# Kernel optimization log

Measured on AMD Instinct MI355X. Metric: run time of the kernel, lower is better.

## Reference

```python
import jax, jax.numpy as jnp
import numpy as np

NUM_EXPERTS = 64
TOP_K = 8
ALPHA = 0.001


def setup_inputs() -> dict:
    key = jax.random.key(0)
    k1, k2 = jax.random.split(key)
    hidden_states = jax.random.normal(k1, (16384, 2048), dtype=jnp.float32)
    # nn.Linear(D, E) weight has shape (E, D); init ~ N(0, 1/sqrt(D))
    weight = jax.random.normal(k2, (NUM_EXPERTS, 2048), dtype=jnp.float32) / jnp.sqrt(2048.0)
    return {"hidden_states": hidden_states, "weight": weight}


def reference(hidden_states, weight):
    # Router logits: (N, E)
    logits = jnp.einsum("nd,ed->ne", hidden_states, weight)
    scores = jax.nn.softmax(logits, axis=-1)

    # top-k (lax.top_k returns sorted values; torch used sorted=False, same set)
    topk_weights, topk_indices = jax.lax.top_k(scores, TOP_K)  # (N, K)
    topk_weights = topk_weights / jnp.sum(topk_weights, axis=-1, keepdims=True)

    # Aux load-balancing loss (training path). Instead of materializing a
    # (N, K, E) one-hot tensor, count tokens per expert with a scatter-add.
    num_tokens = hidden_states.shape[0]
    counts = jnp.zeros((NUM_EXPERTS,), dtype=jnp.float32).at[topk_indices.ravel()].add(1.0)
    tokens_per_expert = counts / (num_tokens * TOP_K)
    mean_prob = jnp.mean(scores, axis=0)  # (E,)
    aux_loss = ALPHA * NUM_EXPERTS * jnp.sum(tokens_per_expert * mean_prob)

    return topk_weights, topk_indices, aux_loss
```

## Files before the change

kernel.cpp:

```cpp
#include <hip/hip_runtime.h>
#include <hip/hip_bf16.h>

#define N_TOKENS 16384
#define DIM      2048
#define NEXP     64
#define TOPK     8
#define LOSCALE  2048.0f
#define NBLOCKS  512
#define TOKPB    32
#define LSTRIDE  66
#define NREP     32
#define NCHUNKS  64
#define NROUNDS  16
#define SROW     264

typedef _Float16 half8   __attribute__((ext_vector_type(8)));
typedef float    floatx4 __attribute__((ext_vector_type(4)));

__global__ __launch_bounds__(256) void wprep_kernel(const float* __restrict__ W,
                                                    _Float16* __restrict__ Whi,
                                                    _Float16* __restrict__ Wlo) {
    int i = blockIdx.x * 256 + threadIdx.x;
    float w = W[i];
    _Float16 h = (_Float16)w;
    Whi[i] = h;
    Wlo[i] = (_Float16)((w - (float)h) * LOSCALE);
}

__device__ __forceinline__ void split2x8(const float4& f0, const float4& f1,
                                         half8& H, half8& L) {
    float v[8] = {f0.x, f0.y, f0.z, f0.w, f1.x, f1.y, f1.z, f1.w};
    #pragma unroll
    for (int j = 0; j < 8; ++j) {
        _Float16 h = (_Float16)v[j];
        H[j] = h;
        L[j] = (_Float16)((v[j] - (float)h) * LOSCALE);
    }
}

__device__ __forceinline__ void split_write(_Float16* sw,
                                            const float4& f0, const float4& f1,
                                            const float4& f2, const float4& f3) {
    half8 h, l;
    split2x8(f0, f1, h, l);
    *(half8*)(sw)      = h;
    *(half8*)(sw + 8)  = l;
    split2x8(f2, f3, h, l);
    *(half8*)(sw + 16) = h;
    *(half8*)(sw + 24) = l;
}

__global__ __launch_bounds__(256) void moe_kernel(const float* __restrict__ A,
                                                  const _Float16* __restrict__ Whi,
                                                  const _Float16* __restrict__ Wlo,
                                                  float* __restrict__ out_w,
                                                  float* __restrict__ out_i,
                                                  float* __restrict__ out_aux,
                                                  float* __restrict__ cnt_ws,
                                                  float* __restrict__ sp_ws,
                                                  unsigned int* __restrict__ ticket) {
    __shared__ _Float16 stage[2][TOKPB][SROW];
    __shared__ float    xch[TOKPB * LSTRIDE];
    __shared__ float    s_cnt[NEXP];
    __shared__ float    s_sp[NEXP];
    __shared__ int      s_last;

    const int tid   = threadIdx.x;
    const int lane  = tid & 63;
    const int wv    = tid >> 6;
    const int row16 = lane & 15;
    const int quad  = lane >> 4;
    const int tbase = blockIdx.x * TOKPB;

    if (tid < NEXP) { s_cnt[tid] = 0.f; s_sp[tid] = 0.f; }

    const int srow = tid >> 3;
    const int sseg = tid & 7;
    const float* Ap = A + (size_t)(tbase + srow) * DIM + sseg * 16;
    _Float16* sw0 = &stage[0][0][0] + srow * SROW + (2 * sseg) * 16;
    _Float16* sw1 = &stage[1][0][0] + srow * SROW + (2 * sseg) * 16;

    const _Float16* bhp = Whi + (size_t)(wv * 16 + row16) * DIM + quad * 8;
    const _Float16* blp = Wlo + (size_t)(wv * 16 + row16) * DIM + quad * 8;

    floatx4 acc0[2] = {};
    floatx4 acc1[2] = {};

#define BODY(I_, BH_, BL_)                                                    \
    do {                                                                      \
        int _off = row16 * SROW + ((I_) * 4 + quad) * 16;                     \
        half8 _a0 = *(const half8*)(sb + _off);                               \
        half8 _l0 = *(const half8*)(sb + _off + 8);                           \
        half8 _a1 = *(const half8*)(sb + _off + 16 * SROW);                   \
        half8 _l1 = *(const half8*)(sb + _off + 16 * SROW + 8);               \
        acc0[0] = __builtin_amdgcn_mfma_f32_16x16x32_f16(_a0, BH_, acc0[0], 0, 0, 0); \
        acc1[0] = __builtin_amdgcn_mfma_f32_16x16x32_f16(_a0, BL_, acc1[0], 0, 0, 0); \
        acc1[0] = __builtin_amdgcn_mfma_f32_16x16x32_f16(_l0, BH_, acc1[0], 0, 0, 0); \
        acc0[1] = __builtin_amdgcn_mfma_f32_16x16x32_f16(_a1, BH_, acc0[1], 0, 0, 0); \
        acc1[1] = __builtin_amdgcn_mfma_f32_16x16x32_f16(_a1, BL_, acc1[1], 0, 0, 0); \
        acc1[1] = __builtin_amdgcn_mfma_f32_16x16x32_f16(_l1, BH_, acc1[1], 0, 0, 0); \
    } while (0)

    half8 b0h = *(const half8*)(bhp + 0 * 32), b0l = *(const half8*)(blp + 0 * 32);
    half8 b1h = *(const half8*)(bhp + 1 * 32), b1l = *(const half8*)(blp + 1 * 32);
    half8 b2h = *(const half8*)(bhp + 2 * 32), b2l = *(const half8*)(blp + 2 * 32);
    half8 b3h = *(const half8*)(bhp + 3 * 32), b3l = *(const half8*)(blp + 3 * 32);

    {
        float4 f0 = *(const float4*)(Ap + 0);
        float4 f1 = *(const float4*)(Ap + 4);
        float4 f2 = *(const float4*)(Ap + 8);
        float4 f3 = *(const float4*)(Ap + 12);
        split_write(sw0, f0, f1, f2, f3);
    }
    __syncthreads();

    for (int r = 0; r < NROUNDS; ++r) {
        float4 g0, g1, g2, g3;
        if (r < NROUNDS - 1) {
            const float* p = Ap + (r + 1) * 128;
            g0 = *(const float4*)(p);
            g1 = *(const float4*)(p + 4);
            g2 = *(const float4*)(p + 8);
            g3 = *(const float4*)(p + 12);
        }
        const _Float16* sb = &stage[r & 1][0][0];
        const int c = 4 * r;

        BODY(0, b0h, b0l);
        if (c + 4 < NCHUNKS) { b0h = *(const half8*)(bhp + (c + 4) * 32); b0l = *(const half8*)(blp + (c + 4) * 32); }
        BODY(1, b1h, b1l);
        if (c + 5 < NCHUNKS) { b1h = *(const half8*)(bhp + (c + 5) * 32); b1l = *(const half8*)(blp + (c + 5) * 32); }
        BODY(2, b2h, b2l);
        if (c + 6 < NCHUNKS) { b2h = *(const half8*)(bhp + (c + 6) * 32); b2l = *(const half8*)(blp + (c + 6) * 32); }
        BODY(3, b3h, b3l);
        if (c + 7 < NCHUNKS) { b3h = *(const half8*)(bhp + (c + 7) * 32); b3l = *(const half8*)(blp + (c + 7) * 32); }

        if (r < NROUNDS - 1) split_write((r & 1) ? sw0 : sw1, g0, g1, g2, g3);
        __syncthreads();
    }

    const float inv = 1.0f / LOSCALE;
    #pragma unroll
    for (int mt = 0; mt < 2; ++mt)
        #pragma unroll
        for (int reg = 0; reg < 4; ++reg) {
            int tok = mt * 16 + quad * 4 + reg;
            xch[tok * LSTRIDE + wv * 16 + row16] = acc0[mt][reg] + acc1[mt][reg] * inv;
        }
    __syncthreads();

    float sp = 0.f, cnt = 0.f;
    for (int i = 0; i < 8; ++i) {
        int t = wv * 8 + i;
        float lg = xch[t * LSTRIDE + lane];

        float m = lg;
        #pragma unroll
        for (int off = 32; off; off >>= 1) m = fmaxf(m, __shfl_xor(m, off));
        float e = expf(lg - m);
        float ssum = e;
        #pragma unroll
        for (int off = 32; off; off >>= 1) ssum += __shfl_xor(ssum, off);
        float score = e / ssum;
        sp += score;

        int rank = 0;
        #pragma unroll
        for (int j = 0; j < 64; ++j) {
            float sj = __shfl(score, j);
            rank += (sj > score) || (sj == score && j < lane);
        }
        bool sel = rank < TOPK;

        float v = sel ? score : 0.f;
        #pragma unroll
        for (int off = 32; off; off >>= 1) v += __shfl_xor(v, off);

        if (sel) {
            out_w[(size_t)(tbase + t) * TOPK + rank] = score / v;
            out_i[(size_t)(tbase + t) * TOPK + rank] = (float)lane;
            cnt += 1.f;
        }
    }

    atomicAdd(&s_sp[lane], sp);
    atomicAdd(&s_cnt[lane], cnt);
    __syncthreads();
    const int rep = (blockIdx.x & (NREP - 1)) * NEXP;
    if (tid < 64)       atomicAdd(&cnt_ws[rep + tid], s_cnt[tid]);
    else if (tid < 128) atomicAdd(&sp_ws[rep + tid - 64], s_sp[tid - 64]);

    __threadfence();
    __syncthreads();
    if (tid == 0)
        s_last = (atomicAdd(ticket, 1u) == (unsigned)(gridDim.x - 1));
    __syncthreads();
    if (s_last && tid < 64) {
        float c = 0.f, p = 0.f;
        #pragma unroll
        for (int rr = 0; rr < NREP; ++rr) {
            c += atomicAdd(&cnt_ws[rr * NEXP + tid], 0.f);
            p += atomicAdd(&sp_ws [rr * NEXP + tid], 0.f);
        }
        float v = (c / (float)(N_TOKENS * TOPK)) * (p / (float)N_TOKENS);
        #pragma unroll
        for (int off = 32; off; off >>= 1) v += __shfl_xor(v, off);
        if (tid == 0) out_aux[0] = 0.001f * (float)NEXP * v;
    }
}

extern "C" void kernel_launch(void* const* d_in, const int* in_sizes, int n_in,
                              void* d_out, int out_size, void* d_ws, size_t ws_size,
                              hipStream_t stream) {
    const float* A = (const float*)d_in[0];
    const float* W = (const float*)d_in[1];
    float* out = (float*)d_out;

    _Float16*     whi    = (_Float16*)d_ws;
    _Float16*     wlo    = whi + (size_t)NEXP * DIM;
    float*        cnt_ws = (float*)(wlo + (size_t)NEXP * DIM);
    float*        sp_ws  = cnt_ws + (size_t)NREP * NEXP;
    unsigned int* ticket = (unsigned int*)(sp_ws + (size_t)NREP * NEXP);

    hipMemsetAsync(cnt_ws, 0, 2 * NREP * NEXP * sizeof(float) + sizeof(unsigned int), stream);

    hipLaunchKernelGGL(wprep_kernel, dim3(NEXP * DIM / 256), dim3(256), 0, stream,
                       W, whi, wlo);

    float* out_w = out;
    float* out_i = out + (size_t)N_TOKENS * TOPK;
    float* out_a = out + 2 * (size_t)N_TOKENS * TOPK;

    hipLaunchKernelGGL(moe_kernel, dim3(NBLOCKS), dim3(256), 0, stream,
                       A, whi, wlo, out_w, out_i, out_a, cnt_ws, sp_ws, ticket);
}
```

Before: 247.0 us.

## Stream fp32 activations directly to LDS with triple-buffered async loads

Replaces the register-staged load-split-store path with global_load_lds (direct-to-LDS) copies into a three-deep fp32 ring buffer, using an XOR swizzle to avoid bank conflicts. The hi/lo fp16 split now happens after reading from LDS, right before the MFMAs. Manual vmcnt waits and raw s_barrier calls replace __syncthreads. The goal is to overlap global loads with compute two rounds ahead and free registers. In exchange, LDS traffic doubles because fp32 is stored instead of the fp16 pair, and the split work is repeated per wave. The hand-counted waitcnt values are fragile.

Measured after the change: 256.6 us. 1.04x slower.

```diff
diff --git a/kernel.cpp b/kernel.cpp
--- a/kernel.cpp
+++ b/kernel.cpp
@@ -10,9 +10,9 @@
 #define TOKPB    32
 #define LSTRIDE  66
 #define NREP     32
-#define NCHUNKS  64
 #define NROUNDS  16
-#define SROW     264
+#define NBUF     3
+#define BUFSZ    (TOKPB * 128)
 
 typedef _Float16 half8   __attribute__((ext_vector_type(8)));
 typedef float    floatx4 __attribute__((ext_vector_type(4)));
@@ -27,27 +27,25 @@
     Wlo[i] = (_Float16)((w - (float)h) * LOSCALE);
 }
 
-__device__ __forceinline__ void split2x8(const float4& f0, const float4& f1,
-                                         half8& H, half8& L) {
-    float v[8] = {f0.x, f0.y, f0.z, f0.w, f1.x, f1.y, f1.z, f1.w};
-    #pragma unroll
-    for (int j = 0; j < 8; ++j) {
-        _Float16 h = (_Float16)v[j];
-        H[j] = h;
-        L[j] = (_Float16)((v[j] - (float)h) * LOSCALE);
-    }
-}
-
-__device__ __forceinline__ void split_write(_Float16* sw,
-                                            const float4& f0, const float4& f1,
-                                            const float4& f2, const float4& f3) {
-    half8 h, l;
-    split2x8(f0, f1, h, l);
-    *(half8*)(sw)      = h;
-    *(half8*)(sw + 8)  = l;
-    split2x8(f2, f3, h, l);
-    *(half8*)(sw + 16) = h;
-    *(half8*)(sw + 24) = l;
+__device__ __forceinline__ void gl_lds16(const float* src, float* lds_base, int byteoff) {
+    __builtin_amdgcn_global_load_lds(
+        (const __attribute__((address_space(1))) unsigned int*)src,
+        (__attribute__((address_space(3))) unsigned int*)((char*)lds_base + byteoff),
+        16, 0, 0);
+}
+
+__device__ __forceinline__ void split8(const floatx4& f0, const floatx4& f1,
+                                       half8& H, half8& L) {
+    #pragma unroll
+    for (int j = 0; j < 4; ++j) {
+        _Float16 h = (_Float16)f0[j];
+        H[j] = h; L[j] = (_Float16)((f0[j] - (float)h) * LOSCALE);
+    }
+    #pragma unroll
+    for (int j = 0; j < 4; ++j) {
+        _Float16 h = (_Float16)f1[j];
+        H[4 + j] = h; L[4 + j] = (_Float16)((f1[j] - (float)h) * LOSCALE);
+    }
 }
 
 __global__ __launch_bounds__(256) void moe_kernel(const float* __restrict__ A,
@@ -59,11 +57,11 @@
                                                   float* __restrict__ cnt_ws,
                                                   float* __restrict__ sp_ws,
                                                   unsigned int* __restrict__ ticket) {
-    __shared__ _Float16 stage[2][TOKPB][SROW];
-    __shared__ float    xch[TOKPB * LSTRIDE];
-    __shared__ float    s_cnt[NEXP];
-    __shared__ float    s_sp[NEXP];
-    __shared__ int      s_last;
+    __shared__ float stage[NBUF][BUFSZ];
+    __shared__ float xch[TOKPB * LSTRIDE];
+    __shared__ float s_cnt[NEXP];
+    __shared__ float s_sp[NEXP];
+    __shared__ int   s_last;
 
     const int tid   = threadIdx.x;
     const int lane  = tid & 63;
@@ -74,11 +72,13 @@
 
     if (tid < NEXP) { s_cnt[tid] = 0.f; s_sp[tid] = 0.f; }
 
-    const int srow = tid >> 3;
-    const int sseg = tid & 7;
-    const float* Ap = A + (size_t)(tbase + srow) * DIM + sseg * 16;
-    _Float16* sw0 = &stage[0][0][0] + srow * SROW + (2 * sseg) * 16;
-    _Float16* sw1 = &stage[1][0][0] + srow * SROW + (2 * sseg) * 16;
+    const float* asrc[4];
+    #pragma unroll
+    for (int j = 0; j < 4; ++j) {
+        int tok  = (wv * 4 + j) * 2 + (lane >> 5);
+        int colb = ((lane & 31) * 16) ^ ((tok & 7) << 4);
+        asrc[j] = (const float*)((const char*)(A + (size_t)(tbase + tok) * DIM) + colb);
+    }
 
     const _Float16* bhp = Whi + (size_t)(wv * 16 + row16) * DIM + quad * 8;
     const _Float16* blp = Wlo + (size_t)(wv * 16 + row16) * DIM + quad * 8;
@@ -86,58 +86,68 @@
     floatx4 acc0[2] = {};
     floatx4 acc1[2] = {};
 
-#define BODY(I_, BH_, BL_)                                                    \
-    do {                                                                      \
-        int _off = row16 * SROW + ((I_) * 4 + quad) * 16;                     \
-        half8 _a0 = *(const half8*)(sb + _off);                               \
-        half8 _l0 = *(const half8*)(sb + _off + 8);                           \
-        half8 _a1 = *(const half8*)(sb + _off + 16 * SROW);                   \
-        half8 _l1 = *(const half8*)(sb + _off + 16 * SROW + 8);               \
-        acc0[0] = __builtin_amdgcn_mfma_f32_16x16x32_f16(_a0, BH_, acc0[0], 0, 0, 0); \
-        acc1[0] = __builtin_amdgcn_mfma_f32_16x16x32_f16(_a0, BL_, acc1[0], 0, 0, 0); \
-        acc1[0] = __builtin_amdgcn_mfma_f32_16x16x32_f16(_l0, BH_, acc1[0], 0, 0, 0); \
-        acc0[1] = __builtin_amdgcn_mfma_f32_16x16x32_f16(_a1, BH_, acc0[1], 0, 0, 0); \
-        acc1[1] = __builtin_amdgcn_mfma_f32_16x16x32_f16(_a1, BL_, acc1[1], 0, 0, 0); \
-        acc1[1] = __builtin_amdgcn_mfma_f32_16x16x32_f16(_l1, BH_, acc1[1], 0, 0, 0); \
-    } while (0)
-
-    half8 b0h = *(const half8*)(bhp + 0 * 32), b0l = *(const half8*)(blp + 0 * 32);
-    half8 b1h = *(const half8*)(bhp + 1 * 32), b1l = *(const half8*)(blp + 1 * 32);
-    half8 b2h = *(const half8*)(bhp + 2 * 32), b2l = *(const half8*)(blp + 2 * 32);
-    half8 b3h = *(const half8*)(bhp + 3 * 32), b3l = *(const half8*)(blp + 3 * 32);
-
-    {
-        float4 f0 = *(const float4*)(Ap + 0);
-        float4 f1 = *(const float4*)(Ap + 4);
-        float4 f2 = *(const float4*)(Ap + 8);
-        float4 f3 = *(const float4*)(Ap + 12);
-        split_write(sw0, f0, f1, f2, f3);
-    }
-    __syncthreads();
-
+    const int c0 = (quad * 8) ^ ((row16 & 7) * 4);
+
+    #pragma unroll
+    for (int j = 0; j < 4; ++j) gl_lds16(asrc[j],       &stage[0][0], (wv * 4 + j) * 1024);
+    #pragma unroll
+    for (int j = 0; j < 4; ++j) gl_lds16(asrc[j] + 128, &stage[1][0], (wv * 4 + j) * 1024);
+
+    half8 bh[4], bl[4];
+    #pragma unroll
+    for (int c = 0; c < 4; ++c) {
+        bh[c] = *(const half8*)(bhp + c * 32);
+        bl[c] = *(const half8*)(blp + c * 32);
+    }
+    asm volatile("s_waitcnt vmcnt(12)" ::: "memory");
+    __builtin_amdgcn_sched_barrier(0);
+    __builtin_amdgcn_s_barrier();
+    __builtin_amdgcn_sched_barrier(0);
+
+    #pragma unroll
     for (int r = 0; r < NROUNDS; ++r) {
-        float4 g0, g1, g2, g3;
+        const float* rb = &stage[r % 3][0];
+
+        if (r < NROUNDS - 2) {
+            #pragma unroll
+            for (int j = 0; j < 4; ++j)
+                gl_lds16(asrc[j] + (r + 2) * 128, &stage[(r + 2) % 3][0], (wv * 4 + j) * 1024);
+        }
+
+        #pragma unroll
+        for (int I = 0; I < 4; ++I) {
+            const float* p0 = rb + row16 * 128 + I * 32;
+            floatx4 f0 = *(const floatx4*)(p0 + c0);
+            floatx4 f1 = *(const floatx4*)(p0 + (c0 ^ 4));
+            half8 ah, al; split8(f0, f1, ah, al);
+            acc0[0] = __builtin_amdgcn_mfma_f32_16x16x32_f16(ah, bh[I], acc0[0], 0, 0, 0);
+            acc1[0] = __builtin_amdgcn_mfma_f32_16x16x32_f16(ah, bl[I], acc1[0], 0, 0, 0);
+            acc1[0] = __builtin_amdgcn_mfma_f32_16x16x32_f16(al, bh[I], acc1[0], 0, 0, 0);
+
+            const float* p1 = rb + (16 + row16) * 128 + I * 32;
+            f0 = *(const floatx4*)(p1 + c0);
+            f1 = *(const floatx4*)(p1 + (c0 ^ 4));
+            split8(f0, f1, ah, al);
+            acc0[1] = __builtin_amdgcn_mfma_f32_16x16x32_f16(ah, bh[I], acc0[1], 0, 0, 0);
+            acc1[1] = __builtin_amdgcn_mfma_f32_16x16x32_f16(ah, bl[I], acc1[1], 0, 0, 0);
+            acc1[1] = __builtin_amdgcn_mfma_f32_16x16x32_f16(al, bh[I], acc1[1], 0, 0, 0);
+
+            if (r < NROUNDS - 1) {
+                bh[I] = *(const half8*)(bhp + ((r + 1) * 4 + I) * 32);
+                bl[I] = *(const half8*)(blp + ((r + 1) * 4 + I) * 32);
+            }
+        }
+
+        if (r < NROUNDS - 2) {
+            asm volatile("s_waitcnt vmcnt(12)" ::: "memory");
+        } else if (r == NROUNDS - 2) {
+            asm volatile("s_waitcnt vmcnt(8)" ::: "memory");
+        }
         if (r < NROUNDS - 1) {
-            const float* p = Ap + (r + 1) * 128;
-            g0 = *(const float4*)(p);
-            g1 = *(const float4*)(p + 4);
-            g2 = *(const float4*)(p + 8);
-            g3 = *(const float4*)(p + 12);
-        }
-        const _Float16* sb = &stage[r & 1][0][0];
-        const int c = 4 * r;
-
-        BODY(0, b0h, b0l);
-        if (c + 4 < NCHUNKS) { b0h = *(const half8*)(bhp + (c + 4) * 32); b0l = *(const half8*)(blp + (c + 4) * 32); }
-        BODY(1, b1h, b1l);
-        if (c + 5 < NCHUNKS) { b1h = *(const half8*)(bhp + (c + 5) * 32); b1l = *(const half8*)(blp + (c + 5) * 32); }
-        BODY(2, b2h, b2l);
-        if (c + 6 < NCHUNKS) { b2h = *(const half8*)(bhp + (c + 6) * 32); b2l = *(const half8*)(blp + (c + 6) * 32); }
-        BODY(3, b3h, b3l);
-        if (c + 7 < NCHUNKS) { b3h = *(const half8*)(bhp + (c + 7) * 32); b3l = *(const half8*)(blp + (c + 7) * 32); }
-
-        if (r < NROUNDS - 1) split_write((r & 1) ? sw0 : sw1, g0, g1, g2, g3);
-        __syncthreads();
+            __builtin_amdgcn_sched_barrier(0);
+            __builtin_amdgcn_s_barrier();
+            __builtin_amdgcn_sched_barrier(0);
+        }
     }
 
     const float inv = 1.0f / LOSCALE;
```

## Split K across two wave groups with 512-thread blocks and separate aux kernel

Applied to the files above, without the earlier changes.

Blocks grow to 512 threads, with each group of four waves handling half of each 256-wide K round. Partial logits from the two halves are summed in shared memory, which is reused from the staging buffer. Staging now splits hi and lo halves into separate regions and halves the number of rounds. The last-block ticket reduction is replaced by a small separate aux kernel, which removes the threadfence and atomic ticket at the cost of an extra launch. The larger block may lower occupancy and adds a partial-sum exchange.

Result: faster. 219.2 us (-11.2%).

```diff
diff --git a/kernel.cpp b/kernel.cpp
--- a/kernel.cpp
+++ b/kernel.cpp
@@ -10,9 +10,9 @@
 #define TOKPB    32
 #define LSTRIDE  66
 #define NREP     32
-#define NCHUNKS  64
-#define NROUNDS  16
-#define SROW     264
+#define KROUND   256
+#define NR       8
+#define SROW     528
 
 typedef _Float16 half8   __attribute__((ext_vector_type(8)));
 typedef float    floatx4 __attribute__((ext_vector_type(4)));
@@ -38,122 +38,122 @@
     }
 }
 
-__device__ __forceinline__ void split_write(_Float16* sw,
+__device__ __forceinline__ void split_write(_Float16* swh, _Float16* swl,
                                             const float4& f0, const float4& f1,
                                             const float4& f2, const float4& f3) {
     half8 h, l;
     split2x8(f0, f1, h, l);
-    *(half8*)(sw)      = h;
-    *(half8*)(sw + 8)  = l;
+    *(half8*)(swh)     = h;
+    *(half8*)(swl)     = l;
     split2x8(f2, f3, h, l);
-    *(half8*)(sw + 16) = h;
-    *(half8*)(sw + 24) = l;
-}
-
-__global__ __launch_bounds__(256) void moe_kernel(const float* __restrict__ A,
+    *(half8*)(swh + 8) = h;
+    *(half8*)(swl + 8) = l;
+}
+
+__global__ __launch_bounds__(512) void moe_kernel(const float* __restrict__ A,
                                                   const _Float16* __restrict__ Whi,
                                                   const _Float16* __restrict__ Wlo,
                                                   float* __restrict__ out_w,
                                                   float* __restrict__ out_i,
-                                                  float* __restrict__ out_aux,
                                                   float* __restrict__ cnt_ws,
-                                                  float* __restrict__ sp_ws,
-                                                  unsigned int* __restrict__ ticket) {
+                                                  float* __restrict__ sp_ws) {
     __shared__ _Float16 stage[2][TOKPB][SROW];
-    __shared__ float    xch[TOKPB * LSTRIDE];
     __shared__ float    s_cnt[NEXP];
     __shared__ float    s_sp[NEXP];
-    __shared__ int      s_last;
 
     const int tid   = threadIdx.x;
     const int lane  = tid & 63;
     const int wv    = tid >> 6;
+    const int es    = wv & 3;
+    const int kh    = wv >> 2;
     const int row16 = lane & 15;
     const int quad  = lane >> 4;
     const int tbase = blockIdx.x * TOKPB;
 
     if (tid < NEXP) { s_cnt[tid] = 0.f; s_sp[tid] = 0.f; }
 
-    const int srow = tid >> 3;
-    const int sseg = tid & 7;
-    const float* Ap = A + (size_t)(tbase + srow) * DIM + sseg * 16;
-    _Float16* sw0 = &stage[0][0][0] + srow * SROW + (2 * sseg) * 16;
-    _Float16* sw1 = &stage[1][0][0] + srow * SROW + (2 * sseg) * 16;
-
-    const _Float16* bhp = Whi + (size_t)(wv * 16 + row16) * DIM + quad * 8;
-    const _Float16* blp = Wlo + (size_t)(wv * 16 + row16) * DIM + quad * 8;
+    const int sr = tid >> 4;
+    const int ss = tid & 15;
+    const float* Ap = A + (size_t)(tbase + sr) * DIM + ss * 16;
+    _Float16* swh0 = &stage[0][sr][0] + ss * 16;
+    _Float16* swh1 = &stage[1][sr][0] + ss * 16;
+
+    const _Float16* bhp = Whi + (size_t)(es * 16 + row16) * DIM + kh * 128 + quad * 8;
+    const _Float16* blp = Wlo + (size_t)(es * 16 + row16) * DIM + kh * 128 + quad * 8;
 
     floatx4 acc0[2] = {};
     floatx4 acc1[2] = {};
-
-#define BODY(I_, BH_, BL_)                                                    \
-    do {                                                                      \
-        int _off = row16 * SROW + ((I_) * 4 + quad) * 16;                     \
-        half8 _a0 = *(const half8*)(sb + _off);                               \
-        half8 _l0 = *(const half8*)(sb + _off + 8);                           \
-        half8 _a1 = *(const half8*)(sb + _off + 16 * SROW);                   \
-        half8 _l1 = *(const half8*)(sb + _off + 16 * SROW + 8);               \
-        acc0[0] = __builtin_amdgcn_mfma_f32_16x16x32_f16(_a0, BH_, acc0[0], 0, 0, 0); \
-        acc1[0] = __builtin_amdgcn_mfma_f32_16x16x32_f16(_a0, BL_, acc1[0], 0, 0, 0); \
-        acc1[0] = __builtin_amdgcn_mfma_f32_16x16x32_f16(_l0, BH_, acc1[0], 0, 0, 0); \
-        acc0[1] = __builtin_amdgcn_mfma_f32_16x16x32_f16(_a1, BH_, acc0[1], 0, 0, 0); \
-        acc1[1] = __builtin_amdgcn_mfma_f32_16x16x32_f16(_a1, BL_, acc1[1], 0, 0, 0); \
-        acc1[1] = __builtin_amdgcn_mfma_f32_16x16x32_f16(_l1, BH_, acc1[1], 0, 0, 0); \
-    } while (0)
-
-    half8 b0h = *(const half8*)(bhp + 0 * 32), b0l = *(const half8*)(blp + 0 * 32);
-    half8 b1h = *(const half8*)(bhp + 1 * 32), b1l = *(const half8*)(blp + 1 * 32);
-    half8 b2h = *(const half8*)(bhp + 2 * 32), b2l = *(const half8*)(blp + 2 * 32);
-    half8 b3h = *(const half8*)(bhp + 3 * 32), b3l = *(const half8*)(blp + 3 * 32);
+    half8 bh[4], bl[4];
 
     {
-        float4 f0 = *(const float4*)(Ap + 0);
+        float4 f0 = *(const float4*)(Ap);
         float4 f1 = *(const float4*)(Ap + 4);
         float4 f2 = *(const float4*)(Ap + 8);
         float4 f3 = *(const float4*)(Ap + 12);
-        split_write(sw0, f0, f1, f2, f3);
+        split_write(swh0, swh0 + 256, f0, f1, f2, f3);
+    }
+    #pragma unroll
+    for (int c = 0; c < 4; ++c) {
+        bh[c] = *(const half8*)(bhp + c * 32);
+        bl[c] = *(const half8*)(blp + c * 32);
     }
     __syncthreads();
 
-    for (int r = 0; r < NROUNDS; ++r) {
+    for (int r = 0; r < NR; ++r) {
         float4 g0, g1, g2, g3;
-        if (r < NROUNDS - 1) {
-            const float* p = Ap + (r + 1) * 128;
+        if (r < NR - 1) {
+            const float* p = Ap + (r + 1) * KROUND;
             g0 = *(const float4*)(p);
             g1 = *(const float4*)(p + 4);
             g2 = *(const float4*)(p + 8);
             g3 = *(const float4*)(p + 12);
         }
         const _Float16* sb = &stage[r & 1][0][0];
-        const int c = 4 * r;
-
-        BODY(0, b0h, b0l);
-        if (c + 4 < NCHUNKS) { b0h = *(const half8*)(bhp + (c + 4) * 32); b0l = *(const half8*)(blp + (c + 4) * 32); }
-        BODY(1, b1h, b1l);
-        if (c + 5 < NCHUNKS) { b1h = *(const half8*)(bhp + (c + 5) * 32); b1l = *(const half8*)(blp + (c + 5) * 32); }
-        BODY(2, b2h, b2l);
-        if (c + 6 < NCHUNKS) { b2h = *(const half8*)(bhp + (c + 6) * 32); b2l = *(const half8*)(blp + (c + 6) * 32); }
-        BODY(3, b3h, b3l);
-        if (c + 7 < NCHUNKS) { b3h = *(const half8*)(bhp + (c + 7) * 32); b3l = *(const half8*)(blp + (c + 7) * 32); }
-
-        if (r < NROUNDS - 1) split_write((r & 1) ? sw0 : sw1, g0, g1, g2, g3);
+
+        #pragma unroll
+        for (int c = 0; c < 4; ++c) {
+            const int k0 = kh * 128 + c * 32 + quad * 8;
+            const _Float16* p0 = sb + row16 * SROW;
+            const _Float16* p1 = sb + (16 + row16) * SROW;
+            half8 a0h = *(const half8*)(p0 + k0);
+            half8 a0l = *(const half8*)(p0 + 256 + k0);
+            half8 a1h = *(const half8*)(p1 + k0);
+            half8 a1l = *(const half8*)(p1 + 256 + k0);
+            acc0[0] = __builtin_amdgcn_mfma_f32_16x16x32_f16(a0h, bh[c], acc0[0], 0, 0, 0);
+            acc1[0] = __builtin_amdgcn_mfma_f32_16x16x32_f16(a0h, bl[c], acc1[0], 0, 0, 0);
+            acc1[0] = __builtin_amdgcn_mfma_f32_16x16x32_f16(a0l, bh[c], acc1[0], 0, 0, 0);
+            acc0[1] = __builtin_amdgcn_mfma_f32_16x16x32_f16(a1h, bh[c], acc0[1], 0, 0, 0);
+            acc1[1] = __builtin_amdgcn_mfma_f32_16x16x32_f16(a1h, bl[c], acc1[1], 0, 0, 0);
+            acc1[1] = __builtin_amdgcn_mfma_f32_16x16x32_f16(a1l, bh[c], acc1[1], 0, 0, 0);
+            if (r < NR - 1) {
+                bh[c] = *(const half8*)(bhp + (r + 1) * KROUND + c * 32);
+                bl[c] = *(const half8*)(blp + (r + 1) * KROUND + c * 32);
+            }
+        }
+
+        if (r < NR - 1) {
+            _Float16* swh = (r & 1) ? swh0 : swh1;
+            split_write(swh, swh + 256, g0, g1, g2, g3);
+        }
         __syncthreads();
     }
 
+    float* xch = (float*)&stage[0][0][0];
     const float inv = 1.0f / LOSCALE;
     #pragma unroll
     for (int mt = 0; mt < 2; ++mt)
         #pragma unroll
         for (int reg = 0; reg < 4; ++reg) {
             int tok = mt * 16 + quad * 4 + reg;
-            xch[tok * LSTRIDE + wv * 16 + row16] = acc0[mt][reg] + acc1[mt][reg] * inv;
+            xch[(kh * TOKPB + tok) * LSTRIDE + es * 16 + row16] =
+                acc0[mt][reg] + acc1[mt][reg] * inv;
         }
     __syncthreads();
 
     float sp = 0.f, cnt = 0.f;
-    for (int i = 0; i < 8; ++i) {
-        int t = wv * 8 + i;
-        float lg = xch[t * LSTRIDE + lane];
+    for (int i = 0; i < 4; ++i) {
+        int t = wv * 4 + i;
+        float lg = xch[t * LSTRIDE + lane] + xch[(TOKPB + t) * LSTRIDE + lane];
 
         float m = lg;
         #pragma unroll
@@ -190,24 +190,22 @@
     const int rep = (blockIdx.x & (NREP - 1)) * NEXP;
     if (tid < 64)       atomicAdd(&cnt_ws[rep + tid], s_cnt[tid]);
     else if (tid < 128) atomicAdd(&sp_ws[rep + tid - 64], s_sp[tid - 64]);
-
-    __threadfence();
-    __syncthreads();
-    if (tid == 0)
-        s_last = (atomicAdd(ticket, 1u) == (unsigned)(gridDim.x - 1));
-    __syncthreads();
-    if (s_last && tid < 64) {
-        float c = 0.f, p = 0.f;
-        #pragma unroll
-        for (int rr = 0; rr < NREP; ++rr) {
-            c += atomicAdd(&cnt_ws[rr * NEXP + tid], 0.f);
-            p += atomicAdd(&sp_ws [rr * NEXP + tid], 0.f);
-        }
-        float v = (c / (float)(N_TOKENS * TOPK)) * (p / (float)N_TOKENS);
-        #pragma unroll
-        for (int off = 32; off; off >>= 1) v += __shfl_xor(v, off);
-        if (tid == 0) out_aux[0] = 0.001f * (float)NEXP * v;
-    }
+}
+
+__global__ __launch_bounds__(64) void aux_kernel(const float* __restrict__ cnt_ws,
+                                                 const float* __restrict__ sp_ws,
+                                                 float* __restrict__ out_aux) {
+    int tid = threadIdx.x;
+    float c = 0.f, p = 0.f;
+    #pragma unroll
+    for (int r = 0; r < NREP; ++r) {
+        c += cnt_ws[r * NEXP + tid];
+        p += sp_ws[r * NEXP + tid];
+    }
+    float v = (c / (float)(N_TOKENS * TOPK)) * (p / (float)N_TOKENS);
+    #pragma unroll
+    for (int off = 32; off; off >>= 1) v += __shfl_xor(v, off);
+    if (tid == 0) out_aux[0] = 0.001f * (float)NEXP * v;
 }
 
 extern "C" void kernel_launch(void* const* d_in, const int* in_sizes, int n_in,
@@ -217,13 +215,12 @@
     const float* W = (const float*)d_in[1];
     float* out = (float*)d_out;
 
-    _Float16*     whi    = (_Float16*)d_ws;
-    _Float16*     wlo    = whi + (size_t)NEXP * DIM;
-    float*        cnt_ws = (float*)(wlo + (size_t)NEXP * DIM);
-    float*        sp_ws  = cnt_ws + (size_t)NREP * NEXP;
-    unsigned int* ticket = (unsigned int*)(sp_ws + (size_t)NREP * NEXP);
-
-    hipMemsetAsync(cnt_ws, 0, 2 * NREP * NEXP * sizeof(float) + sizeof(unsigned int), stream);
+    _Float16* whi    = (_Float16*)d_ws;
+    _Float16* wlo    = whi + (size_t)NEXP * DIM;
+    float*    cnt_ws = (float*)(wlo + (size_t)NEXP * DIM);
+    float*    sp_ws  = cnt_ws + (size_t)NREP * NEXP;
+
+    hipMemsetAsync(cnt_ws, 0, 2 * NREP * NEXP * sizeof(float), stream);
 
     hipLaunchKernelGGL(wprep_kernel, dim3(NEXP * DIM / 256), dim3(256), 0, stream,
                        W, whi, wlo);
@@ -232,6 +229,9 @@
     float* out_i = out + (size_t)N_TOKENS * TOPK;
     float* out_a = out + 2 * (size_t)N_TOKENS * TOPK;
 
-    hipLaunchKernelGGL(moe_kernel, dim3(NBLOCKS), dim3(256), 0, stream,
-                       A, whi, wlo, out_w, out_i, out_a, cnt_ws, sp_ws, ticket);
-}
+    hipLaunchKernelGGL(moe_kernel, dim3(NBLOCKS), dim3(512), 0, stream,
+                       A, whi, wlo, out_w, out_i, cnt_ws, sp_ws);
+
+    hipLaunchKernelGGL(aux_kernel, dim3(1), dim3(64), 0, stream,
+                       cnt_ws, sp_ws, out_a);
+}
```
